# Kernel optimization log

Hardware: AMD Instinct MI355X
Metric: run time of the kernel (lower is better)

## Reference

```python
import jax, jax.numpy as jnp
import numpy as np
import math

B, S, D = 1, 4096, 512
H, KVH, DH = 8, 4, 64
DH2 = DH // 2
M = int(math.isqrt(S))           # product-key grid side, S == M*M
K = 8                            # top_k
ROPE_BASE = 10000.0


def rope_cos_sin(seq_len, dh, base):
    inv_freq = 1.0 / (base ** (jnp.arange(0, dh, 2, dtype=jnp.float32) / dh))
    t = jnp.arange(seq_len, dtype=jnp.float32)
    freqs = jnp.outer(t, inv_freq)                      # (S, dh/2)
    emb = jnp.concatenate([freqs, freqs], axis=-1)      # (S, dh)
    return jnp.cos(emb), jnp.sin(emb)


def apply_rope(x, cos, sin):
    # x: (B, H, S, dh); half-split rotation (llama-style)
    dh2 = x.shape[-1] // 2
    rot = jnp.concatenate([-x[..., dh2:], x[..., :dh2]], axis=-1)
    return x * cos + rot * sin


def setup_inputs() -> dict:
    key = jax.random.key(0)
    ks = jax.random.split(key, 5)
    s = 0.02
    x = jax.random.normal(ks[0], (B, S, D), dtype=jnp.float32)
    Wq = jax.random.normal(ks[1], (H * DH, D), dtype=jnp.float32) * s
    Wk = jax.random.normal(ks[2], (KVH * DH, D), dtype=jnp.float32) * s
    Wv = jax.random.normal(ks[3], (KVH * DH, D), dtype=jnp.float32) * s
    Wo = jax.random.normal(ks[4], (D, H * DH), dtype=jnp.float32) * s
    return {"x": x, "Wq": Wq, "Wk": Wk, "Wv": Wv, "Wo": Wo}


def reference(x, Wq, Wk, Wv, Wo):
    b, s, d = x.shape
    cos, sin = rope_cos_sin(s, DH, ROPE_BASE)
    q = (x @ Wq.T).reshape(b, s, H, DH).transpose(0, 2, 1, 3)      # (B,H,S,DH)
    k = (x @ Wk.T).reshape(b, s, KVH, DH).transpose(0, 2, 1, 3)    # (B,KVH,S,DH)
    v = (x @ Wv.T).reshape(b, s, KVH, DH).transpose(0, 2, 1, 3)
    q = apply_rope(q, cos, sin)
    k = apply_rope(k, cos, sin)
    rep = H // KVH                                                 # GQA repeat_kv
    k = jnp.repeat(k, rep, axis=1)                                 # (B,H,S,DH)
    v = jnp.repeat(v, rep, axis=1)

    # factorized product keys: sum over grid rows / cols
    kg = k.reshape(b, H, M, M, DH)
    k1 = kg[..., :DH2].sum(axis=-2)                                # (B,H,M,DH2)
    k2 = kg[..., DH2:].sum(axis=-3)                                # (B,H,M,DH2)
    q1, q2 = q[..., :DH2], q[..., DH2:]

    def topk_sel(qh, kh):  # qh: (S,DH2), kh: (M,DH2)
        scores = qh @ kh.T                                         # (S,M)
        _, idx = jax.lax.top_k(scores, K)                          # (S,K)
        return kh[idx], idx                                        # (S,K,DH2), (S,K)

    sel2 = jax.vmap(jax.vmap(topk_sel))
    k1v, i1 = sel2(q1, k1)                                         # (B,H,S,K,DH2)
    k2v, i2 = sel2(q2, k2)

    # cross-product candidates: (B,H,S,K,K,DH) -> (B,H,S,K*K,DH)
    c1 = jnp.broadcast_to(k1v[:, :, :, :, None, :], (b, H, s, K, K, DH2))
    c2 = jnp.broadcast_to(k2v[:, :, :, None, :, :], (b, H, s, K, K, DH2))
    cand = jnp.concatenate([c1, c2], axis=-1).reshape(b, H, s, K * K, DH)

    scores_final = jnp.einsum('bhsd,bhscd->bhsc', q, cand)         # (B,H,S,K*K)
    _, sel = jax.lax.top_k(scores_final, K)                        # (B,H,S,K)
    final_k = jnp.take_along_axis(cand, sel[..., None], axis=3)    # (B,H,S,K,DH)

    row = jnp.take_along_axis(i1, sel // K, axis=3)
    col = jnp.take_along_axis(i2, sel % K, axis=3)
    v_idx = row * M + col                                          # (B,H,S,K)
    final_v = jax.vmap(jax.vmap(lambda vb, ib: vb[ib]))(v, v_idx)  # (B,H,S,K,DH)

    attn = jax.nn.softmax(
        jnp.einsum('bhsd,bhskd->bhsk', q, final_k) / math.sqrt(DH), axis=-1)
    o = jnp.einsum('bhsk,bhskd->bhsd', attn, final_v)              # (B,H,S,DH)
    o = o.transpose(0, 2, 1, 3).reshape(b, s, H * DH)
    return o @ Wo.T
```

## Files before the change

kernel.cpp:

```cpp
#include <hip/hip_runtime.h>
#include <math.h>


static constexpr size_t OFF_P1   = 0;
static constexpr size_t OFF_P2   = 4194304;
static constexpr size_t OFF_KB   = 8388608;
static constexpr size_t OFF_V    = 9437184;
static constexpr size_t OFF_COS  = 10485760;
static constexpr size_t OFF_SIN  = 10616832;
static constexpr size_t OFF_K1   = 10747904;
static constexpr size_t OFF_K2   = 10756096;
static constexpr size_t OFF_O    = 10764288;
static constexpr size_t OFF_PACK = 12861440;

#define LDB 132
#define TILE_F (16 * LDB)

__device__ __forceinline__ float rdlane_f(float v, int lane) {
  return __int_as_float(__builtin_amdgcn_readlane(__float_as_int(v), lane));
}

__global__ __launch_bounds__(256) void freq_table_kernel(float* __restrict__ cosT,
    float* __restrict__ sinT) {
  int idx = blockIdx.x * 256 + threadIdx.x;
  int s = idx >> 5;
  int dp = idx & 31;
  double e = (double)dp * (1.0 / 32.0);
  float pf = (float)pow(10000.0, e);
  float invf = 1.0f / pf;
  float argf = __fmul_rn((float)s, invf);
  cosT[idx] = (float)cos((double)argf);
  sinT[idx] = (float)sin((double)argf);
}

__global__ __launch_bounds__(256) void gemm128_qkv(const float* __restrict__ A,
    const float* __restrict__ Wq, const float* __restrict__ Wk,
    const float* __restrict__ Wv, float* __restrict__ C1,
    float* __restrict__ C2) {
  __shared__ float As[2 * TILE_F];
  __shared__ float Bs[2 * TILE_F];
  const int tid = threadIdx.x;
  const int z = blockIdx.z;
  const int k0 = z ? 384 : 0;
  const int k1 = z ? 512 : 384;
  float* __restrict__ C = z ? C2 : C1;
  const int bm = blockIdx.y, bn = blockIdx.x;
  const int lrow = tid >> 1;
  const int lko = (tid & 1) << 3;
  const int ty = tid >> 4;
  const int tx = tid & 15;
  const float* Bbase = (bn < 4) ? (Wq + ((size_t)bn * 128) * 512)
                     : (bn < 6) ? (Wk + ((size_t)(bn - 4) * 128) * 512)
                                : (Wv + ((size_t)(bn - 6) * 128) * 512);
  const float* Ap = A + (size_t)(bm * 128 + lrow) * 512 + lko;
  const float* Bp = Bbase + (size_t)lrow * 512 + lko;
  float acc[8][8] = {{0.f}};
  float4 a0 = *(const float4*)(Ap + k0);
  float4 a1 = *(const float4*)(Ap + k0 + 4);
  float4 b0 = *(const float4*)(Bp + k0);
  float4 b1 = *(const float4*)(Bp + k0 + 4);
  int p = 0;
  for (int kt = k0; kt < k1; kt += 16) {
    float* Asp = As + p * TILE_F;
    float* Bsp = Bs + p * TILE_F;
    Asp[(lko + 0) * LDB + lrow] = a0.x;
    Asp[(lko + 1) * LDB + lrow] = a0.y;
    Asp[(lko + 2) * LDB + lrow] = a0.z;
    Asp[(lko + 3) * LDB + lrow] = a0.w;
    Asp[(lko + 4) * LDB + lrow] = a1.x;
    Asp[(lko + 5) * LDB + lrow] = a1.y;
    Asp[(lko + 6) * LDB + lrow] = a1.z;
    Asp[(lko + 7) * LDB + lrow] = a1.w;
    Bsp[(lko + 0) * LDB + lrow] = b0.x;
    Bsp[(lko + 1) * LDB + lrow] = b0.y;
    Bsp[(lko + 2) * LDB + lrow] = b0.z;
    Bsp[(lko + 3) * LDB + lrow] = b0.w;
    Bsp[(lko + 4) * LDB + lrow] = b1.x;
    Bsp[(lko + 5) * LDB + lrow] = b1.y;
    Bsp[(lko + 6) * LDB + lrow] = b1.z;
    Bsp[(lko + 7) * LDB + lrow] = b1.w;
    __syncthreads();
    if (kt + 16 < k1) {
      a0 = *(const float4*)(Ap + kt + 16);
      a1 = *(const float4*)(Ap + kt + 20);
      b0 = *(const float4*)(Bp + kt + 16);
      b1 = *(const float4*)(Bp + kt + 20);
    }
    #pragma unroll
    for (int k = 0; k < 16; ++k) {
      float4 al = *(const float4*)(&Asp[k * LDB + (ty << 2)]);
      float4 ah = *(const float4*)(&Asp[k * LDB + 64 + (ty << 2)]);
      float4 bl = *(const float4*)(&Bsp[k * LDB + (tx << 2)]);
      float4 bh = *(const float4*)(&Bsp[k * LDB + 64 + (tx << 2)]);
      float af[8] = {al.x, al.y, al.z, al.w, ah.x, ah.y, ah.z, ah.w};
      float bf[8] = {bl.x, bl.y, bl.z, bl.w, bh.x, bh.y, bh.z, bh.w};
      #pragma unroll
      for (int i2 = 0; i2 < 8; ++i2)
        #pragma unroll
        for (int j2 = 0; j2 < 8; ++j2)
          acc[i2][j2] = fmaf(af[i2], bf[j2], acc[i2][j2]);
    }
    p ^= 1;
  }
  #pragma unroll
  for (int i2 = 0; i2 < 8; ++i2) {
    int row = bm * 128 + ((i2 < 4) ? (ty << 2) + i2 : 64 + (ty << 2) + i2 - 4);
    float* Cp = C + (size_t)row * 1024 + bn * 128;
    *(float4*)(Cp + (tx << 2))      = make_float4(acc[i2][0], acc[i2][1], acc[i2][2], acc[i2][3]);
    *(float4*)(Cp + 64 + (tx << 2)) = make_float4(acc[i2][4], acc[i2][5], acc[i2][6], acc[i2][7]);
  }
}

__global__ __launch_bounds__(256) void gemm128_out(const float* __restrict__ A,
    const float* __restrict__ B, float* __restrict__ Cbase, int N) {
  __shared__ float As[2 * TILE_F];
  __shared__ float Bs[2 * TILE_F];
  const int tid = threadIdx.x;
  const int z = blockIdx.z;
  const int k0 = z << 7;
  const int k1 = k0 + 128;
  float* __restrict__ C = Cbase + (size_t)z * ((size_t)4096 * N);
  const int bm = blockIdx.y, bn = blockIdx.x;
  const int lrow = tid >> 1;
  const int lko = (tid & 1) << 3;
  const int ty = tid >> 4;
  const int tx = tid & 15;
  const float* Ap = A + (size_t)(bm * 128 + lrow) * 512 + lko;
  const float* Bp = B + (size_t)(bn * 128 + lrow) * 512 + lko;
  float acc[8][8] = {{0.f}};
  float4 a0 = *(const float4*)(Ap + k0);
  float4 a1 = *(const float4*)(Ap + k0 + 4);
  float4 b0 = *(const float4*)(Bp + k0);
  float4 b1 = *(const float4*)(Bp + k0 + 4);
  int p = 0;
  for (int kt = k0; kt < k1; kt += 16) {
    float* Asp = As + p * TILE_F;
    float* Bsp = Bs + p * TILE_F;
    Asp[(lko + 0) * LDB + lrow] = a0.x;
    Asp[(lko + 1) * LDB + lrow] = a0.y;
    Asp[(lko + 2) * LDB + lrow] = a0.z;
    Asp[(lko + 3) * LDB + lrow] = a0.w;
    Asp[(lko + 4) * LDB + lrow] = a1.x;
    Asp[(lko + 5) * LDB + lrow] = a1.y;
    Asp[(lko + 6) * LDB + lrow] = a1.z;
    Asp[(lko + 7) * LDB + lrow] = a1.w;
    Bsp[(lko + 0) * LDB + lrow] = b0.x;
    Bsp[(lko + 1) * LDB + lrow] = b0.y;
    Bsp[(lko + 2) * LDB + lrow] = b0.z;
    Bsp[(lko + 3) * LDB + lrow] = b0.w;
    Bsp[(lko + 4) * LDB + lrow] = b1.x;
    Bsp[(lko + 5) * LDB + lrow] = b1.y;
    Bsp[(lko + 6) * LDB + lrow] = b1.z;
    Bsp[(lko + 7) * LDB + lrow] = b1.w;
    __syncthreads();
    if (kt + 16 < k1) {
      a0 = *(const float4*)(Ap + kt + 16);
      a1 = *(const float4*)(Ap + kt + 20);
      b0 = *(const float4*)(Bp + kt + 16);
      b1 = *(const float4*)(Bp + kt + 20);
    }
    #pragma unroll
    for (int k = 0; k < 16; ++k) {
      float4 al = *(const float4*)(&Asp[k * LDB + (ty << 2)]);
      float4 ah = *(const float4*)(&Asp[k * LDB + 64 + (ty << 2)]);
      float4 bl = *(const float4*)(&Bsp[k * LDB + (tx << 2)]);
      float4 bh = *(const float4*)(&Bsp[k * LDB + 64 + (tx << 2)]);
      float af[8] = {al.x, al.y, al.z, al.w, ah.x, ah.y, ah.z, ah.w};
      float bf[8] = {bl.x, bl.y, bl.z, bl.w, bh.x, bh.y, bh.z, bh.w};
      #pragma unroll
      for (int i2 = 0; i2 < 8; ++i2)
        #pragma unroll
        for (int j2 = 0; j2 < 8; ++j2)
          acc[i2][j2] = fmaf(af[i2], bf[j2], acc[i2][j2]);
    }
    p ^= 1;
  }
  #pragma unroll
  for (int i2 = 0; i2 < 8; ++i2) {
    int row = bm * 128 + ((i2 < 4) ? (ty << 2) + i2 : 64 + (ty << 2) + i2 - 4);
    float* Cp = C + (size_t)row * N + bn * 128;
    *(float4*)(Cp + (tx << 2))      = make_float4(acc[i2][0], acc[i2][1], acc[i2][2], acc[i2][3]);
    *(float4*)(Cp + 64 + (tx << 2)) = make_float4(acc[i2][4], acc[i2][5], acc[i2][6], acc[i2][7]);
  }
}

__global__ __launch_bounds__(256) void combine4_kernel(const float* __restrict__ o0,
    const float* __restrict__ o1, const float* __restrict__ o2,
    const float* __restrict__ o3, float* __restrict__ out) {
  int i = blockIdx.x * 256 + threadIdx.x;
  out[i] = __fadd_rn(__fadd_rn(__fadd_rn(o0[i], o1[i]), o2[i]), o3[i]);
}

__global__ __launch_bounds__(256) void kv_rope_kernel(const float* __restrict__ p1,
    const float* __restrict__ p2, const float* __restrict__ cosT,
    const float* __restrict__ sinT, float* __restrict__ kb,
    float* __restrict__ vb) {
  int id = blockIdx.x * 256 + threadIdx.x;
  int s = id >> 9;
  int n = 512 + (id & 511);
  int idx = (s << 10) + n;
  float val = __fadd_rn(p1[idx], p2[idx]);
  int d = n & 63;
  if (n < 768) {
    int pidx = idx ^ 32;
    float pv = __fadd_rn(p1[pidx], p2[pidx]);
    float cs = cosT[(s << 5) + (d & 31)];
    float sn = sinT[(s << 5) + (d & 31)];
    float rot = (d < 32) ? -pv : pv;
    float out = __fadd_rn(__fmul_rn(val, cs), __fmul_rn(rot, sn));
    int kvh = (n - 512) >> 6;
    kb[((size_t)(kvh * 4096 + s) << 6) + d] = out;
  } else {
    int kvh = (n - 768) >> 6;
    vb[((size_t)(kvh * 4096 + s) << 6) + d] = val;
  }
}

__global__ __launch_bounds__(256) void k12_np_kernel(const float* __restrict__ kb,
    float* __restrict__ k1t, float* __restrict__ k2t) {
  int id = blockIdx.x * 256 + threadIdx.x;
  int which = id >> 13;
  int rem = id & 8191;
  int kvh = rem >> 11;
  int rem2 = rem & 2047;
  int i = rem2 >> 5;
  int d = rem2 & 31;
  const float* base = kb + ((size_t)(kvh * 4096) << 6);
  if (which == 0) {
    float acc = base[((size_t)(i * 64) << 6) + d];
    for (int c = 1; c < 64; ++c)
      acc = __fadd_rn(acc, base[((size_t)(i * 64 + c) << 6) + d]);
    k1t[(kvh * 64 + i) * 32 + d] = acc;
  } else {
    float acc = base[((size_t)i << 6) + d + 32];
    for (int r = 1; r < 64; ++r)
      acc = __fadd_rn(acc, base[((size_t)(r * 64 + i) << 6) + d + 32]);
    k2t[(kvh * 64 + i) * 32 + d] = acc;
  }
}

__global__ __launch_bounds__(256) void stage1_sel_kernel(
    const float* __restrict__ p1, const float* __restrict__ p2,
    const float* __restrict__ cosT, const float* __restrict__ sinT,
    const float* __restrict__ k1t, const float* __restrict__ k2t,
    unsigned long long* __restrict__ packs) {
  __shared__ float smem[8704];
  float* qs = smem;
  float* kd = smem + 4352;
  const int t = threadIdx.x;
  const int h = blockIdx.y;
  const int s0 = blockIdx.x * 64;
  const int kvh = h >> 1;
  #pragma unroll
  for (int i = 0; i < 16; ++i) {
    int j = t + i * 256;
    int ss = j >> 6, d = j & 63;
    int s = s0 + ss;
    int idx = (s << 10) + (h << 6) + d;
    float val = __fadd_rn(p1[idx], p2[idx]);
    float pv  = __fadd_rn(p1[idx ^ 32], p2[idx ^ 32]);
    float cs = cosT[(s << 5) + (d & 31)];
    float sn = sinT[(s << 5) + (d & 31)];
    float rot = (d < 32) ? -pv : pv;
    qs[d * 68 + ss] = __fadd_rn(__fmul_rn(val, cs), __fmul_rn(rot, sn));
  }
  #pragma unroll
  for (int i = 0; i < 8; ++i) {
    int j = t + i * 256;
    int r = j >> 5, d = j & 31;
    kd[d * 132 + r]      = k1t[(kvh * 64 + r) * 32 + d];
    kd[d * 132 + 64 + r] = k2t[(kvh * 64 + r) * 32 + d];
  }
  __syncthreads();
  const int ty = t >> 4;
  const int tx = t & 15;
  float acc1[4][4] = {{0.f}};
  float acc2[4][4] = {{0.f}};
  #pragma unroll
  for (int dp = 0; dp < 32; ++dp) {
    float4 kv1 = *(const float4*)&kd[dp * 132 + (ty << 2)];
    float4 kv2 = *(const float4*)&kd[dp * 132 + 64 + (ty << 2)];
    float4 q1 = *(const float4*)&qs[dp * 68 + (tx << 2)];
    float4 q2 = *(const float4*)&qs[(32 + dp) * 68 + (tx << 2)];
    float k1f[4] = {kv1.x, kv1.y, kv1.z, kv1.w};
    float k2f[4] = {kv2.x, kv2.y, kv2.z, kv2.w};
    float q1f[4] = {q1.x, q1.y, q1.z, q1.w};
    float q2f[4] = {q2.x, q2.y, q2.z, q2.w};
    #pragma unroll
    for (int i2 = 0; i2 < 4; ++i2)
      #pragma unroll
      for (int j2 = 0; j2 < 4; ++j2) {
        acc1[i2][j2] = fmaf(k1f[i2], q1f[j2], acc1[i2][j2]);
        acc2[i2][j2] = fmaf(k2f[i2], q2f[j2], acc2[i2][j2]);
      }
  }
  __syncthreads();
  float* sct = smem;
  #pragma unroll
  for (int i2 = 0; i2 < 4; ++i2) {
    int r = (ty << 2) + i2;
    *(float4*)&sct[(size_t)r * 68 + (tx << 2)] =
        make_float4(acc1[i2][0], acc1[i2][1], acc1[i2][2], acc1[i2][3]);
    *(float4*)&sct[(size_t)(64 + r) * 68 + (tx << 2)] =
        make_float4(acc2[i2][0], acc2[i2][1], acc2[i2][2], acc2[i2][3]);
  }
  __syncthreads();
  if (t < 128) {
    int set = t >> 6;
    int sq = t & 63;
    const float* p = sct + (size_t)(set << 6) * 68 + sq;
    float top[8];
    int idx[8];
    #pragma unroll
    for (int u = 0; u < 8; ++u) { top[u] = -INFINITY; idx[u] = 0; }
    #pragma unroll
    for (int r = 0; r < 64; ++r) {
      float v = p[(size_t)r * 68];
      int i = r;
      #pragma unroll
      for (int j = 0; j < 8; ++j) {
        bool gt = v > top[j];
        float tv = top[j]; int ti = idx[j];
        top[j] = gt ? v : tv;
        idx[j] = gt ? i : ti;
        v = gt ? tv : v;
        i = gt ? ti : i;
      }
    }
    unsigned long long pp = 0;
    #pragma unroll
    for (int u = 0; u < 8; ++u) pp |= (unsigned long long)idx[u] << (6 * u);
    packs[(((size_t)(h * 4096 + s0 + sq)) << 1) + set] = pp;
  }
}

__device__ __forceinline__ void bitonic64_val_desc(float& v, int lane) {
  #pragma unroll
  for (int k = 2; k <= 64; k <<= 1) {
    #pragma unroll
    for (int j = k >> 1; j >= 1; j >>= 1) {
      float ov = __shfl_xor(v, j, 64);
      bool up = ((lane & k) == 0) == ((lane & j) == 0);
      float mx = fmaxf(v, ov), mn = fminf(v, ov);
      v = up ? mx : mn;
    }
  }
}

__global__ __launch_bounds__(256) void attn_sel2_kernel(
    const ulonglong2* __restrict__ packs, const float* __restrict__ p1,
    const float* __restrict__ p2, const float* __restrict__ cosT,
    const float* __restrict__ sinT, const float* __restrict__ vb,
    const float* __restrict__ k1t, const float* __restrict__ k2t,
    float* __restrict__ ob) {
  const int lane = threadIdx.x & 63;
  const int w = blockIdx.x * 4 + (threadIdx.x >> 6);
  const int h = w >> 12;
  const int s = w & 4095;
  const int kvh = h >> 1;
  ulonglong2 pk = packs[w];
  const unsigned long long pack1 = pk.x, pack2 = pk.y;
  int qidx = (s << 10) + (h << 6) + lane;
  float vraw = __fadd_rn(p1[qidx], p2[qidx]);
  float pv = __shfl_xor(vraw, 32, 64);
  float cs = cosT[(s << 5) + (lane & 31)];
  float sn = sinT[(s << 5) + (lane & 31)];
  float rot = (lane < 32) ? -pv : pv;
  const float qv = __fadd_rn(__fmul_rn(vraw, cs), __fmul_rn(rot, sn));

  int r1 = (int)((pack1 >> (6 * (lane >> 3))) & 63);
  int r2 = (int)((pack2 >> (6 * (lane & 7))) & 63);
  const float* k1p = k1t + (size_t)(kvh * 64 + r1) * 32;
  const float* k2p = k2t + (size_t)(kvh * 64 + r2) * 32;
  float c = 0.f;
  #pragma unroll
  for (int dq = 0; dq < 32; dq += 4) {
    float4 kk = *(const float4*)(k1p + dq);
    c = __fadd_rn(c, __fmul_rn(rdlane_f(qv, dq + 0), kk.x));
    c = __fadd_rn(c, __fmul_rn(rdlane_f(qv, dq + 1), kk.y));
    c = __fadd_rn(c, __fmul_rn(rdlane_f(qv, dq + 2), kk.z));
    c = __fadd_rn(c, __fmul_rn(rdlane_f(qv, dq + 3), kk.w));
  }
  #pragma unroll
  for (int dq = 0; dq < 32; dq += 4) {
    float4 kk = *(const float4*)(k2p + dq);
    c = __fadd_rn(c, __fmul_rn(rdlane_f(qv, 32 + dq + 0), kk.x));
    c = __fadd_rn(c, __fmul_rn(rdlane_f(qv, 32 + dq + 1), kk.y));
    c = __fadd_rn(c, __fmul_rn(rdlane_f(qv, 32 + dq + 2), kk.z));
    c = __fadd_rn(c, __fmul_rn(rdlane_f(qv, 32 + dq + 3), kk.w));
  }
  const float scand = c;
  float v3 = c;
  bitonic64_val_desc(v3, lane);
  float cvs[8]; int ccs[8];
  unsigned long long used = 0;
  #pragma unroll
  for (int t = 0; t < 8; ++t) {
    float tv = rdlane_f(v3, t);
    unsigned long long m = __ballot(scand == tv) & ~used;
    int ix = __ffsll((long long)m) - 1;
    used |= 1ull << ix;
    cvs[t] = tv;
    ccs[t] = ix;
  }
  float y[8];
  #pragma unroll
  for (int t = 0; t < 8; ++t) y[t] = cvs[t] * 0.125f;
  float mx = y[0];
  #pragma unroll
  for (int t = 1; t < 8; ++t) if (y[t] > mx) mx = y[t];
  float e[8];
  #pragma unroll
  for (int t = 0; t < 8; ++t) e[t] = __expf(__fsub_rn(y[t], mx));
  float wsum = __fadd_rn(__fadd_rn(__fadd_rn(e[0], e[1]), __fadd_rn(e[2], e[3])),
                         __fadd_rn(__fadd_rn(e[4], e[5]), __fadd_rn(e[6], e[7])));
  const float* vbh = vb + ((size_t)kvh << 18);
  float o = 0.f;
  #pragma unroll
  for (int t = 0; t < 8; ++t) {
    float att = __fdiv_rn(e[t], wsum);
    int row = (int)((pack1 >> (6 * (ccs[t] >> 3))) & 63);
    int col = (int)((pack2 >> (6 * (ccs[t] & 7))) & 63);
    o = __fadd_rn(o, __fmul_rn(att, vbh[((size_t)(row * 64 + col) << 6) + lane]));
  }
  ob[(size_t)s * 512 + (h << 6) + lane] = o;
}

extern "C" void kernel_launch(void* const* d_in, const int* in_sizes, int n_in,
                              void* d_out, int out_size, void* d_ws, size_t ws_size,
                              hipStream_t stream) {
  const float* x  = (const float*)d_in[0];
  const float* Wq = (const float*)d_in[1];
  const float* Wk = (const float*)d_in[2];
  const float* Wv = (const float*)d_in[3];
  const float* Wo = (const float*)d_in[4];
  float* ws = (float*)d_ws;
  float* p1   = ws + OFF_P1;
  float* p2   = ws + OFF_P2;
  float* kb   = ws + OFF_KB;
  float* vb   = ws + OFF_V;
  float* cosT = ws + OFF_COS;
  float* sinT = ws + OFF_SIN;
  float* k1t  = ws + OFF_K1;
  float* k2t  = ws + OFF_K2;
  float* ob   = ws + OFF_O;
  unsigned long long* packs = (unsigned long long*)(ws + OFF_PACK);
  float* op = ws + OFF_P1;

  freq_table_kernel<<<512, 256, 0, stream>>>(cosT, sinT);
  gemm128_qkv<<<dim3(8, 32, 2), 256, 0, stream>>>(x, Wq, Wk, Wv, p1, p2);
  kv_rope_kernel<<<8192, 256, 0, stream>>>(p1, p2, cosT, sinT, kb, vb);
  k12_np_kernel<<<64, 256, 0, stream>>>(kb, k1t, k2t);
  stage1_sel_kernel<<<dim3(64, 8), 256, 0, stream>>>(p1, p2, cosT, sinT, k1t, k2t, packs);
  attn_sel2_kernel<<<8192, 256, 0, stream>>>((const ulonglong2*)packs, p1, p2,
                                             cosT, sinT, vb, k1t, k2t, ob);
  gemm128_out<<<dim3(4, 32, 4), 256, 0, stream>>>(ob, Wo, op, 512);
  combine4_kernel<<<8192, 256, 0, stream>>>(op, op + 2097152, op + 4194304,
                                            op + 6291456, (float*)d_out);
}
```

Before: 235.5 us.

## Fuse RoPE table generation into QKV GEMM launch and halve per-thread tile

Merges the cos/sin table kernel and the QKV projection GEMM into one launch: the first 512 blocks do the GEMM and the extra 256 blocks build the tables. This removes a launch and lets the double-precision table work overlap with the GEMM. The GEMM block grows to 512 threads, each computing a 4x8 output tile instead of 8x8 and loading one float4 per operand instead of two. That gives more waves to hide latency, at the cost of more LDS traffic per FMA.

New measurement: 236.0 us. No clear change (+0.2%).

```diff
diff --git a/kernel.cpp b/kernel.cpp
--- a/kernel.cpp
+++ b/kernel.cpp
@@ -20,33 +20,35 @@
   return __int_as_float(__builtin_amdgcn_readlane(__float_as_int(v), lane));
 }
 
-__global__ __launch_bounds__(256) void freq_table_kernel(float* __restrict__ cosT,
-    float* __restrict__ sinT) {
-  int idx = blockIdx.x * 256 + threadIdx.x;
-  int s = idx >> 5;
-  int dp = idx & 31;
-  double e = (double)dp * (1.0 / 32.0);
-  float pf = (float)pow(10000.0, e);
-  float invf = 1.0f / pf;
-  float argf = __fmul_rn((float)s, invf);
-  cosT[idx] = (float)cos((double)argf);
-  sinT[idx] = (float)sin((double)argf);
-}
-
-__global__ __launch_bounds__(256) void gemm128_qkv(const float* __restrict__ A,
+__global__ __launch_bounds__(512) void pre_kernel(const float* __restrict__ A,
     const float* __restrict__ Wq, const float* __restrict__ Wk,
     const float* __restrict__ Wv, float* __restrict__ C1,
-    float* __restrict__ C2) {
+    float* __restrict__ C2, float* __restrict__ cosT,
+    float* __restrict__ sinT) {
   __shared__ float As[2 * TILE_F];
   __shared__ float Bs[2 * TILE_F];
+  const int bid = blockIdx.x;
   const int tid = threadIdx.x;
-  const int z = blockIdx.z;
+  if (bid >= 512) {
+    int idx = (bid - 512) * 512 + tid;
+    int s = idx >> 5;
+    int dp = idx & 31;
+    double e = (double)dp * (1.0 / 32.0);
+    float pf = (float)pow(10000.0, e);
+    float invf = 1.0f / pf;
+    float argf = __fmul_rn((float)s, invf);
+    cosT[idx] = (float)cos((double)argf);
+    sinT[idx] = (float)sin((double)argf);
+    return;
+  }
+  const int bn = bid & 7;
+  const int bm = (bid >> 3) & 31;
+  const int z = bid >> 8;
   const int k0 = z ? 384 : 0;
   const int k1 = z ? 512 : 384;
   float* __restrict__ C = z ? C2 : C1;
-  const int bm = blockIdx.y, bn = blockIdx.x;
-  const int lrow = tid >> 1;
-  const int lko = (tid & 1) << 3;
+  const int lrow = tid >> 2;
+  const int lko = (tid & 3) << 2;
   const int ty = tid >> 4;
   const int tx = tid & 15;
   const float* Bbase = (bn < 4) ? (Wq + ((size_t)bn * 128) * 512)
@@ -54,11 +56,9 @@
                                 : (Wv + ((size_t)(bn - 6) * 128) * 512);
   const float* Ap = A + (size_t)(bm * 128 + lrow) * 512 + lko;
   const float* Bp = Bbase + (size_t)lrow * 512 + lko;
-  float acc[8][8] = {{0.f}};
+  float acc[4][8] = {{0.f}};
   float4 a0 = *(const float4*)(Ap + k0);
-  float4 a1 = *(const float4*)(Ap + k0 + 4);
   float4 b0 = *(const float4*)(Bp + k0);
-  float4 b1 = *(const float4*)(Bp + k0 + 4);
   int p = 0;
   for (int kt = k0; kt < k1; kt += 16) {
     float* Asp = As + p * TILE_F;
@@ -67,35 +67,24 @@
     Asp[(lko + 1) * LDB + lrow] = a0.y;
     Asp[(lko + 2) * LDB + lrow] = a0.z;
     Asp[(lko + 3) * LDB + lrow] = a0.w;
-    Asp[(lko + 4) * LDB + lrow] = a1.x;
-    Asp[(lko + 5) * LDB + lrow] = a1.y;
-    Asp[(lko + 6) * LDB + lrow] = a1.z;
-    Asp[(lko + 7) * LDB + lrow] = a1.w;
     Bsp[(lko + 0) * LDB + lrow] = b0.x;
     Bsp[(lko + 1) * LDB + lrow] = b0.y;
     Bsp[(lko + 2) * LDB + lrow] = b0.z;
     Bsp[(lko + 3) * LDB + lrow] = b0.w;
-    Bsp[(lko + 4) * LDB + lrow] = b1.x;
-    Bsp[(lko + 5) * LDB + lrow] = b1.y;
-    Bsp[(lko + 6) * LDB + lrow] = b1.z;
-    Bsp[(lko + 7) * LDB + lrow] = b1.w;
     __syncthreads();
     if (kt + 16 < k1) {
       a0 = *(const float4*)(Ap + kt + 16);
-      a1 = *(const float4*)(Ap + kt + 20);
       b0 = *(const float4*)(Bp + kt + 16);
-      b1 = *(const float4*)(Bp + kt + 20);
     }
     #pragma unroll
     for (int k = 0; k < 16; ++k) {
-      float4 al = *(const float4*)(&Asp[k * LDB + (ty << 2)]);
-      float4 ah = *(const float4*)(&Asp[k * LDB + 64 + (ty << 2)]);
+      float4 av = *(const float4*)(&Asp[k * LDB + (ty << 2)]);
       float4 bl = *(const float4*)(&Bsp[k * LDB + (tx << 2)]);
       float4 bh = *(const float4*)(&Bsp[k * LDB + 64 + (tx << 2)]);
-      float af[8] = {al.x, al.y, al.z, al.w, ah.x, ah.y, ah.z, ah.w};
+      float af[4] = {av.x, av.y, av.z, av.w};
       float bf[8] = {bl.x, bl.y, bl.z, bl.w, bh.x, bh.y, bh.z, bh.w};
       #pragma unroll
-      for (int i2 = 0; i2 < 8; ++i2)
+      for (int i2 = 0; i2 < 4; ++i2)
         #pragma unroll
         for (int j2 = 0; j2 < 8; ++j2)
           acc[i2][j2] = fmaf(af[i2], bf[j2], acc[i2][j2]);
@@ -103,8 +92,8 @@
     p ^= 1;
   }
   #pragma unroll
-  for (int i2 = 0; i2 < 8; ++i2) {
-    int row = bm * 128 + ((i2 < 4) ? (ty << 2) + i2 : 64 + (ty << 2) + i2 - 4);
+  for (int i2 = 0; i2 < 4; ++i2) {
+    int row = bm * 128 + (ty << 2) + i2;
     float* Cp = C + (size_t)row * 1024 + bn * 128;
     *(float4*)(Cp + (tx << 2))      = make_float4(acc[i2][0], acc[i2][1], acc[i2][2], acc[i2][3]);
     *(float4*)(Cp + 64 + (tx << 2)) = make_float4(acc[i2][4], acc[i2][5], acc[i2][6], acc[i2][7]);
@@ -447,8 +436,7 @@
   unsigned long long* packs = (unsigned long long*)(ws + OFF_PACK);
   float* op = ws + OFF_P1;
 
-  freq_table_kernel<<<512, 256, 0, stream>>>(cosT, sinT);
-  gemm128_qkv<<<dim3(8, 32, 2), 256, 0, stream>>>(x, Wq, Wk, Wv, p1, p2);
+  pre_kernel<<<768, 512, 0, stream>>>(x, Wq, Wk, Wv, p1, p2, cosT, sinT);
   kv_rope_kernel<<<8192, 256, 0, stream>>>(p1, p2, cosT, sinT, kb, vb);
   k12_np_kernel<<<64, 256, 0, stream>>>(kb, k1t, k2t);
   stage1_sel_kernel<<<dim3(64, 8), 256, 0, stream>>>(p1, p2, cosT, sinT, k1t, k2t, packs);
```
